# Optimization experiments

Hardware: AMD Instinct MI355X
Metric: run time of the kernel (lower is better)

The kernel has to match this reference:

```python
import jax, jax.numpy as jnp
import numpy as np

N_NODES = 50000
N_EDGES = 1600000
IN_FEAT = 128
HIDDEN = 128
CLASSES = 2


def gin_conv(x, src, dst, W, b, n_nodes):
    # GINConv (eps=0): h_i = mlp(x_i + sum_{j in N(i)} x_j)
    agg = jax.ops.segment_sum(x[src], dst, num_segments=n_nodes)  # [N, F]
    h = x + agg
    return h @ W + b


def setup_inputs() -> dict:
    key = jax.random.key(0)
    ks = jax.random.split(key, 8)
    x = jax.random.normal(ks[0], (N_NODES, IN_FEAT), dtype=jnp.float32)
    edge_index = jax.random.randint(ks[1], (2, N_EDGES), 0, N_NODES, dtype=jnp.int64)
    def lin(k, fan_in, fan_out):
        kw, kb = jax.random.split(k)
        bound = 1.0 / np.sqrt(fan_in)
        W = jax.random.uniform(kw, (fan_in, fan_out), jnp.float32, -bound, bound)
        b = jax.random.uniform(kb, (fan_out,), jnp.float32, -bound, bound)
        return W, b
    W1, b1 = lin(ks[2], IN_FEAT, HIDDEN)
    W2, b2 = lin(ks[3], HIDDEN, HIDDEN)
    W3, b3 = lin(ks[4], HIDDEN, CLASSES)
    return {"x": x, "edge_index": edge_index, "W1": W1, "b1": b1,
            "W2": W2, "b2": b2, "W3": W3, "b3": b3}


def reference(x, edge_index, W1, b1, W2, b2, W3, b3):
    src, dst = edge_index[0], edge_index[1]
    n = x.shape[0]
    h = jax.nn.relu(gin_conv(x, src, dst, W1, b1, n))
    h = jax.nn.relu(gin_conv(h, src, dst, W2, b2, n))
    return gin_conv(h, src, dst, W3, b3, n)
```

## Files before the change

kernel.cpp:

```cpp
#include <hip/hip_runtime.h>

#define NNODES 50000
#define NEDGES 1600000
#define F 128

#define NB 128
#define BSH 391
#define BCAP 13312
#define EPT 10

typedef __attribute__((ext_vector_type(8))) short bf16x8;
typedef __attribute__((ext_vector_type(4))) float f32x4;

__device__ inline unsigned short f2bf(float f) {
    union { float f; unsigned u; } v; v.f = f;
    unsigned r = v.u + 0x7FFF + ((v.u >> 16) & 1);
    return (unsigned short)(r >> 16);
}
__device__ inline float b2f(unsigned short h) {
    union { unsigned u; float f; } a;
    a.u = ((unsigned)h) << 16;
    return a.f;
}

__global__ __launch_bounds__(256) void cvt_bf16(const float4* __restrict__ in,
                                                ushort4* __restrict__ out, int n4) {
    int i = blockIdx.x * blockDim.x + threadIdx.x;
    int stride = gridDim.x * blockDim.x;
    for (; i < n4; i += stride) {
        float4 v = in[i];
        ushort4 o;
        o.x = f2bf(v.x); o.y = f2bf(v.y); o.z = f2bf(v.z); o.w = f2bf(v.w);
        out[i] = o;
    }
}

__global__ __launch_bounds__(256) void wprep2(const float* __restrict__ W1,
                                              const float* __restrict__ W2,
                                              unsigned short* __restrict__ Wf1,
                                              unsigned short* __restrict__ Wf2,
                                              int* __restrict__ gcnt) {
    int id = blockIdx.x * 256 + threadIdx.x;
    if (blockIdx.x == 0 && threadIdx.x < NB) gcnt[threadIdx.x] = 0;
    const float* W = (id < 2048) ? W1 : W2;
    unsigned short* Wf = (id < 2048) ? Wf1 : Wf2;
    id &= 2047;
    const int l = id & 63, nn = (id >> 6) & 7, s = id >> 9;
    const int c = nn * 16 + (l & 15);
    const int k0 = s * 32 + (l >> 4) * 8;
    ushort4 lo, hi;
    lo.x = f2bf(W[(k0 + 0) * F + c]); lo.y = f2bf(W[(k0 + 1) * F + c]);
    lo.z = f2bf(W[(k0 + 2) * F + c]); lo.w = f2bf(W[(k0 + 3) * F + c]);
    hi.x = f2bf(W[(k0 + 4) * F + c]); hi.y = f2bf(W[(k0 + 5) * F + c]);
    hi.z = f2bf(W[(k0 + 6) * F + c]); hi.w = f2bf(W[(k0 + 7) * F + c]);
    ushort4* p = (ushort4*)(Wf + (size_t)id * 8);
    p[0] = lo; p[1] = hi;
}

__global__ __launch_bounds__(256) void bucketA(const int* __restrict__ src,
                                               const int* __restrict__ dst,
                                               unsigned* __restrict__ E1,
                                               int* __restrict__ gcnt) {
    __shared__ unsigned hist[4][NB];
    __shared__ unsigned start[4][NB];
    const int t = threadIdx.x, w = t >> 6;
    for (int i = t; i < 4 * NB; i += 256) ((unsigned*)hist)[i] = 0;
    __syncthreads();
    const int base = blockIdx.x * (256 * EPT);
    unsigned rec[EPT]; int bkt[EPT]; unsigned rnk[EPT];
#pragma unroll
    for (int k = 0; k < EPT; ++k) {
        const int i = base + k * 256 + t;
        const int s = src[i], d = dst[i];
        const int b = d / BSH;
        rec[k] = ((unsigned)s << 9) | (unsigned)(d - b * BSH);
        bkt[k] = b;
        rnk[k] = atomicAdd(&hist[w][b], 1u);
    }
    __syncthreads();
    if (t < NB) {
        const unsigned h0 = hist[0][t], h1 = hist[1][t], h2 = hist[2][t], h3 = hist[3][t];
        const unsigned tot = h0 + h1 + h2 + h3;
        const unsigned g = tot ? (unsigned)atomicAdd(&gcnt[t], (int)tot) : 0u;
        start[0][t] = g;
        start[1][t] = g + h0;
        start[2][t] = g + h0 + h1;
        start[3][t] = g + h0 + h1 + h2;
    }
    __syncthreads();
#pragma unroll
    for (int k = 0; k < EPT; ++k) {
        const unsigned p = start[w][bkt[k]] + rnk[k];
        if (p < BCAP) E1[(size_t)bkt[k] * BCAP + p] = rec[k];
    }
}

__global__ __launch_bounds__(256) void bucketB(const unsigned* __restrict__ E1,
                                               const int* __restrict__ gcnt,
                                               int* __restrict__ off,
                                               unsigned short* __restrict__ ssrc) {
    __shared__ int cnt[BSH];
    __shared__ int cur[BSH];
    __shared__ int wtot[4];
    __shared__ int bst[NB];
    const int b = blockIdx.x, t = threadIdx.x;
    if (t < 64) {
        const int a0 = gcnt[t * 2], a1 = gcnt[t * 2 + 1];
        const int s = a0 + a1;
        int inc = s;
#pragma unroll
        for (int o = 1; o <= 32; o <<= 1) {
            int u = __shfl_up(inc, o);
            if (t >= o) inc += u;
        }
        bst[t * 2] = inc - s;
        bst[t * 2 + 1] = inc - s + a0;
    }
    for (int i = t; i < BSH; i += 256) cnt[i] = 0;
    __syncthreads();
    const int ne = min(gcnt[b], BCAP);
    const int ebase = bst[b];
    const unsigned* E = E1 + (size_t)b * BCAP;
    for (int i = t; i < ne; i += 256) atomicAdd(&cnt[E[i] & 511], 1);
    __syncthreads();
    const int i0 = t * 2, i1 = t * 2 + 1;
    const int a0 = (i0 < BSH) ? cnt[i0] : 0;
    const int a1 = (i1 < BSH) ? cnt[i1] : 0;
    const int s = a0 + a1;
    int inc = s;
    const int lane = t & 63, w = t >> 6;
#pragma unroll
    for (int o = 1; o <= 32; o <<= 1) {
        int u = __shfl_up(inc, o);
        if (lane >= o) inc += u;
    }
    if (lane == 63) wtot[w] = inc;
    __syncthreads();
    int woff = 0;
    for (int k = 0; k < w; ++k) woff += wtot[k];
    const int excl = woff + inc - s;
    if (i0 < BSH) {
        cur[i0] = excl;
        const int n = b * BSH + i0;
        if (n < NNODES) off[n] = ebase + excl;
    }
    if (i1 < BSH) {
        cur[i1] = excl + a0;
        const int n = b * BSH + i1;
        if (n < NNODES) off[n] = ebase + excl + a0;
    }
    if (b == NB - 1 && t == 0) off[NNODES] = NEDGES;
    __syncthreads();
    for (int i = t; i < ne; i += 256) {
        const unsigned rec = E[i];
        const int r = atomicAdd(&cur[rec & 511], 1);
        ssrc[ebase + r] = (unsigned short)(rec >> 9);
    }
}

__global__ __launch_bounds__(256) void agg_mlp(const unsigned short* __restrict__ h,
                                               const int* __restrict__ off,
                                               const unsigned short* __restrict__ ssrc,
                                               const unsigned short* __restrict__ Wfrag,
                                               const float* __restrict__ bias,
                                               unsigned short* __restrict__ out,
                                               int n, int relu) {
    __shared__ unsigned short Sl[4][16][128];
    const int w = threadIdx.x >> 6, lane = threadIdx.x & 63;
    const int nbase = blockIdx.x * 64 + w * 16;
    const int half = lane >> 5, l32 = lane & 31;

    for (int m = 0; m < 16; ++m) {
        const int node = nbase + m;
        float a0 = 0.f, a1 = 0.f, a2 = 0.f, a3 = 0.f;
        if (node < n) {
            const int e0 = off[node], e1 = off[node + 1];
            if (half == 0) {
                const ushort4 sv = *(const ushort4*)(h + (size_t)node * F + l32 * 4);
                a0 = b2f(sv.x); a1 = b2f(sv.y); a2 = b2f(sv.z); a3 = b2f(sv.w);
            }
            for (int eb = e0; eb < e1; eb += 64) {
                const int cnt = min(64, e1 - eb);
                const int myidx = (eb + lane < e1) ? (int)ssrc[eb + lane] : 0;
                int j = 0;
                for (; j + 8 <= cnt; j += 8) {
                    const int s0 = __shfl(myidx, j + 0 + half);
                    const int s1 = __shfl(myidx, j + 2 + half);
                    const int s2 = __shfl(myidx, j + 4 + half);
                    const int s3 = __shfl(myidx, j + 6 + half);
                    const ushort4 v0 = *(const ushort4*)(h + (size_t)s0 * F + l32 * 4);
                    const ushort4 v1 = *(const ushort4*)(h + (size_t)s1 * F + l32 * 4);
                    const ushort4 v2 = *(const ushort4*)(h + (size_t)s2 * F + l32 * 4);
                    const ushort4 v3 = *(const ushort4*)(h + (size_t)s3 * F + l32 * 4);
                    a0 += (b2f(v0.x) + b2f(v1.x)) + (b2f(v2.x) + b2f(v3.x));
                    a1 += (b2f(v0.y) + b2f(v1.y)) + (b2f(v2.y) + b2f(v3.y));
                    a2 += (b2f(v0.z) + b2f(v1.z)) + (b2f(v2.z) + b2f(v3.z));
                    a3 += (b2f(v0.w) + b2f(v1.w)) + (b2f(v2.w) + b2f(v3.w));
                }
                for (; j < cnt; j += 2) {
                    const int s = __shfl(myidx, min(j + half, cnt - 1));
                    if (j + half < cnt) {
                        const ushort4 v = *(const ushort4*)(h + (size_t)s * F + l32 * 4);
                        a0 += b2f(v.x); a1 += b2f(v.y); a2 += b2f(v.z); a3 += b2f(v.w);
                    }
                }
            }
        }
        a0 += __shfl_xor(a0, 32); a1 += __shfl_xor(a1, 32);
        a2 += __shfl_xor(a2, 32); a3 += __shfl_xor(a3, 32);
        if (half == 0) {
            ushort4 wbv;
            wbv.x = f2bf(a0); wbv.y = f2bf(a1); wbv.z = f2bf(a2); wbv.w = f2bf(a3);
            *(ushort4*)(&Sl[w][m][(l32 * 4) ^ ((m & 7) << 3)]) = wbv;
        }
    }

    const int r16 = lane & 15, hi = lane >> 4;
    f32x4 acc[8];
#pragma unroll
    for (int i = 0; i < 8; ++i) acc[i] = (f32x4){0.f, 0.f, 0.f, 0.f};
#pragma unroll
    for (int s = 0; s < 4; ++s) {
        const bf16x8 a = *(const bf16x8*)(&Sl[w][r16][(s * 32 + hi * 8) ^ ((r16 & 7) << 3)]);
#pragma unroll
        for (int nn = 0; nn < 8; ++nn) {
            const bf16x8 b = *(const bf16x8*)(Wfrag + ((size_t)(s * 8 + nn) * 64 + lane) * 8);
            acc[nn] = __builtin_amdgcn_mfma_f32_16x16x32_bf16(a, b, acc[nn], 0, 0, 0);
        }
    }
#pragma unroll
    for (int nn = 0; nn < 8; ++nn) {
        const int col = nn * 16 + r16;
        const float bv = bias[col];
#pragma unroll
        for (int r = 0; r < 4; ++r) {
            const int row = nbase + hi * 4 + r;
            if (row < n) {
                float v = acc[nn][r] + bv;
                if (relu) v = fmaxf(v, 0.f);
                out[(size_t)row * F + col] = f2bf(v);
            }
        }
    }
}

__global__ __launch_bounds__(256) void head_t(const unsigned short* __restrict__ Hb,
                                              const float4* __restrict__ W3,
                                              float2* __restrict__ y, int n) {
    const int wid = (blockIdx.x * blockDim.x + threadIdx.x) >> 6;
    const int lane = threadIdx.x & 63;
    if (wid >= n) return;
    const unsigned short* hp = Hb + (size_t)wid * F + lane * 2;
    const float hx = b2f(hp[0]), hy = b2f(hp[1]);
    const float4 w = W3[lane];
    float a0 = hx * w.x + hy * w.z;
    float a1 = hx * w.y + hy * w.w;
#pragma unroll
    for (int o = 32; o; o >>= 1) {
        a0 += __shfl_xor(a0, o);
        a1 += __shfl_xor(a1, o);
    }
    if (lane == 0) y[wid] = make_float2(a0, a1);
}

__global__ __launch_bounds__(256) void agg3(const float2* __restrict__ y,
                                            const int* __restrict__ off,
                                            const unsigned short* __restrict__ ssrc,
                                            const float* __restrict__ b3,
                                            float2* __restrict__ out, int n) {
    const int i = blockIdx.x * blockDim.x + threadIdx.x;
    if (i >= n) return;
    float2 acc = y[i];
    const int e1 = off[i + 1];
    for (int e = off[i]; e < e1; ++e) {
        const float2 v = y[ssrc[e]];
        acc.x += v.x;
        acc.y += v.y;
    }
    out[i] = make_float2(acc.x + b3[0], acc.y + b3[1]);
}

extern "C" void kernel_launch(void* const* d_in, const int* in_sizes, int n_in,
                              void* d_out, int out_size, void* d_ws, size_t ws_size,
                              hipStream_t stream) {
    const float* x  = (const float*)d_in[0];
    const int* ei   = (const int*)d_in[1];
    const int* src  = ei;
    const int* dst  = ei + NEDGES;
    const float* W1 = (const float*)d_in[2];
    const float* b1 = (const float*)d_in[3];
    const float* W2 = (const float*)d_in[4];
    const float* b2 = (const float*)d_in[5];
    const float* W3 = (const float*)d_in[6];
    const float* b3 = (const float*)d_in[7];
    float* out = (float*)d_out;

    char* ws = (char*)d_ws;
    const size_t featB = (size_t)NNODES * F * 2;
    unsigned short* xb = (unsigned short*)ws;
    unsigned short* Hb = (unsigned short*)(ws + featB);
    char* p = ws + 2 * featB;
    float* y3 = (float*)p;                 p += (size_t)NNODES * 2 * 4 + 256;
    unsigned short* Wf1 = (unsigned short*)p; p += 2048 * 8 * 2;
    unsigned short* Wf2 = (unsigned short*)p; p += 2048 * 8 * 2;
    unsigned* E1 = (unsigned*)p;           p += (size_t)NB * BCAP * 4;
    int* gcnt = (int*)p;                   p += NB * 4 + 256;
    int* off = (int*)p;                    p += (size_t)(NNODES + 1) * 4 + 256;
    unsigned short* ssrc = (unsigned short*)p;

    cvt_bf16<<<1024, 256, 0, stream>>>((const float4*)x, (ushort4*)xb, NNODES * F / 4);
    wprep2<<<16, 256, 0, stream>>>(W1, W2, Wf1, Wf2, gcnt);

    bucketA<<<NEDGES / (256 * EPT), 256, 0, stream>>>(src, dst, E1, gcnt);
    bucketB<<<NB, 256, 0, stream>>>(E1, gcnt, off, ssrc);

    const int fusedBlocks = (NNODES + 63) / 64;

    agg_mlp<<<fusedBlocks, 256, 0, stream>>>(xb, off, ssrc, Wf1, b1, Hb, NNODES, 1);
    agg_mlp<<<fusedBlocks, 256, 0, stream>>>(Hb, off, ssrc, Wf2, b2, xb, NNODES, 1);

    head_t<<<(NNODES + 3) / 4, 256, 0, stream>>>(xb, (const float4*)W3, (float2*)y3, NNODES);
    agg3<<<(NNODES + 255) / 256, 256, 0, stream>>>((const float2*)y3, off, ssrc, b3, (float2*)out, NNODES);
}
```

Measured before the change: 315.7 us.

## Split wavefront halves across two nodes and use single-wave blocks in agg_mlp

Each 64-lane wave now aggregates two nodes at once, one per 32-lane half, instead of splitting one node's edges between the halves and reducing them with a cross-half shuffle. The inner gather loop is unrolled to 8 loads per half, and blocks shrink to one wave covering 16 nodes, so there are four times as many blocks. The aim is to drop the cross-half reduction and wasted tail lanes, raise memory-level parallelism and balance the load at finer grain. In exchange, the two halves can diverge when their nodes have different degrees, and register use rises from the wider unroll.

```diff
diff --git a/kernel.cpp b/kernel.cpp
--- a/kernel.cpp
+++ b/kernel.cpp
@@ -158,61 +158,66 @@
     }
 }
 
-__global__ __launch_bounds__(256) void agg_mlp(const unsigned short* __restrict__ h,
-                                               const int* __restrict__ off,
-                                               const unsigned short* __restrict__ ssrc,
-                                               const unsigned short* __restrict__ Wfrag,
-                                               const float* __restrict__ bias,
-                                               unsigned short* __restrict__ out,
-                                               int n, int relu) {
-    __shared__ unsigned short Sl[4][16][128];
-    const int w = threadIdx.x >> 6, lane = threadIdx.x & 63;
-    const int nbase = blockIdx.x * 64 + w * 16;
+__global__ __launch_bounds__(64) void agg_mlp(const unsigned short* __restrict__ h,
+                                              const int* __restrict__ off,
+                                              const unsigned short* __restrict__ ssrc,
+                                              const unsigned short* __restrict__ Wfrag,
+                                              const float* __restrict__ bias,
+                                              unsigned short* __restrict__ out,
+                                              int n, int relu) {
+    __shared__ unsigned short Sl[16][128];
+    const int lane = threadIdx.x;
+    const int nbase = blockIdx.x * 16;
     const int half = lane >> 5, l32 = lane & 31;
 
-    for (int m = 0; m < 16; ++m) {
-        const int node = nbase + m;
+    for (int m = 0; m < 16; m += 2) {
+        const int row = m + half;
+        const int node = nbase + row;
         float a0 = 0.f, a1 = 0.f, a2 = 0.f, a3 = 0.f;
         if (node < n) {
             const int e0 = off[node], e1 = off[node + 1];
-            if (half == 0) {
-                const ushort4 sv = *(const ushort4*)(h + (size_t)node * F + l32 * 4);
-                a0 = b2f(sv.x); a1 = b2f(sv.y); a2 = b2f(sv.z); a3 = b2f(sv.w);
-            }
-            for (int eb = e0; eb < e1; eb += 64) {
-                const int cnt = min(64, e1 - eb);
-                const int myidx = (eb + lane < e1) ? (int)ssrc[eb + lane] : 0;
+            const ushort4 sv = *(const ushort4*)(h + (size_t)node * F + l32 * 4);
+            a0 = b2f(sv.x); a1 = b2f(sv.y); a2 = b2f(sv.z); a3 = b2f(sv.w);
+            for (int eb = e0; eb < e1; eb += 32) {
+                const int cnt = min(32, e1 - eb);
+                const int myidx = (eb + l32 < e1) ? (int)ssrc[eb + l32] : 0;
                 int j = 0;
                 for (; j + 8 <= cnt; j += 8) {
-                    const int s0 = __shfl(myidx, j + 0 + half);
-                    const int s1 = __shfl(myidx, j + 2 + half);
-                    const int s2 = __shfl(myidx, j + 4 + half);
-                    const int s3 = __shfl(myidx, j + 6 + half);
+                    const int s0 = __shfl(myidx, j + 0, 32);
+                    const int s1 = __shfl(myidx, j + 1, 32);
+                    const int s2 = __shfl(myidx, j + 2, 32);
+                    const int s3 = __shfl(myidx, j + 3, 32);
+                    const int s4 = __shfl(myidx, j + 4, 32);
+                    const int s5 = __shfl(myidx, j + 5, 32);
+                    const int s6 = __shfl(myidx, j + 6, 32);
+                    const int s7 = __shfl(myidx, j + 7, 32);
                     const ushort4 v0 = *(const ushort4*)(h + (size_t)s0 * F + l32 * 4);
                     const ushort4 v1 = *(const ushort4*)(h + (size_t)s1 * F + l32 * 4);
                     const ushort4 v2 = *(const ushort4*)(h + (size_t)s2 * F + l32 * 4);
                     const ushort4 v3 = *(const ushort4*)(h + (size_t)s3 * F + l32 * 4);
-                    a0 += (b2f(v0.x) + b2f(v1.x)) + (b2f(v2.x) + b2f(v3.x));
-                    a1 += (b2f(v0.y) + b2f(v1.y)) + (b2f(v2.y) + b2f(v3.y));
-                    a2 += (b2f(v0.z) + b2f(v1.z)) + (b2f(v2.z) + b2f(v3.z));
-                    a3 += (b2f(v0.w) + b2f(v1.w)) + (b2f(v2.w) + b2f(v3.w));
+                    const ushort4 v4 = *(const ushort4*)(h + (size_t)s4 * F + l32 * 4);
+                    const ushort4 v5 = *(const ushort4*)(h + (size_t)s5 * F + l32 * 4);
+                    const ushort4 v6 = *(const ushort4*)(h + (size_t)s6 * F + l32 * 4);
+                    const ushort4 v7 = *(const ushort4*)(h + (size_t)s7 * F + l32 * 4);
+                    a0 += ((b2f(v0.x) + b2f(v1.x)) + (b2f(v2.x) + b2f(v3.x))) +
+                          ((b2f(v4.x) + b2f(v5.x)) + (b2f(v6.x) + b2f(v7.x)));
+                    a1 += ((b2f(v0.y) + b2f(v1.y)) + (b2f(v2.y) + b2f(v3.y))) +
+                          ((b2f(v4.y) + b2f(v5.y)) + (b2f(v6.y) + b2f(v7.y)));
+                    a2 += ((b2f(v0.z) + b2f(v1.z)) + (b2f(v2.z) + b2f(v3.z))) +
+                          ((b2f(v4.z) + b2f(v5.z)) + (b2f(v6.z) + b2f(v7.z)));
+                    a3 += ((b2f(v0.w) + b2f(v1.w)) + (b2f(v2.w) + b2f(v3.w))) +
+                          ((b2f(v4.w) + b2f(v5.w)) + (b2f(v6.w) + b2f(v7.w)));
                 }
-                for (; j < cnt; j += 2) {
-                    const int s = __shfl(myidx, min(j + half, cnt - 1));
-                    if (j + half < cnt) {
-                        const ushort4 v = *(const ushort4*)(h + (size_t)s * F + l32 * 4);
-                        a0 += b2f(v.x); a1 += b2f(v.y); a2 += b2f(v.z); a3 += b2f(v.w);
-                    }
+                for (; j < cnt; ++j) {
+                    const int s = __shfl(myidx, j, 32);
+                    const ushort4 v = *(const ushort4*)(h + (size_t)s * F + l32 * 4);
+                    a0 += b2f(v.x); a1 += b2f(v.y); a2 += b2f(v.z); a3 += b2f(v.w);
                 }
             }
         }
-        a0 += __shfl_xor(a0, 32); a1 += __shfl_xor(a1, 32);
-        a2 += __shfl_xor(a2, 32); a3 += __shfl_xor(a3, 32);
-        if (half == 0) {
-            ushort4 wbv;
-            wbv.x = f2bf(a0); wbv.y = f2bf(a1); wbv.z = f2bf(a2); wbv.w = f2bf(a3);
-            *(ushort4*)(&Sl[w][m][(l32 * 4) ^ ((m & 7) << 3)]) = wbv;
-        }
+        ushort4 wbv;
+        wbv.x = f2bf(a0); wbv.y = f2bf(a1); wbv.z = f2bf(a2); wbv.w = f2bf(a3);
+        *(ushort4*)(&Sl[row][(l32 * 4) ^ ((row & 7) << 3)]) = wbv;
     }
 
     const int r16 = lane & 15, hi = lane >> 4;
@@ -221,7 +226,7 @@
     for (int i = 0; i < 8; ++i) acc[i] = (f32x4){0.f, 0.f, 0.f, 0.f};
 #pragma unroll
     for (int s = 0; s < 4; ++s) {
-        const bf16x8 a = *(const bf16x8*)(&Sl[w][r16][(s * 32 + hi * 8) ^ ((r16 & 7) << 3)]);
+        const bf16x8 a = *(const bf16x8*)(&Sl[r16][(s * 32 + hi * 8) ^ ((r16 & 7) << 3)]);
 #pragma unroll
         for (int nn = 0; nn < 8; ++nn) {
             const bf16x8 b = *(const bf16x8*)(Wfrag + ((size_t)(s * 8 + nn) * 64 + lane) * 8);
@@ -314,10 +319,10 @@
     bucketA<<<NEDGES / (256 * EPT), 256, 0, stream>>>(src, dst, E1, gcnt);
     bucketB<<<NB, 256, 0, stream>>>(E1, gcnt, off, ssrc);
 
-    const int fusedBlocks = (NNODES + 63) / 64;
-
-    agg_mlp<<<fusedBlocks, 256, 0, stream>>>(xb, off, ssrc, Wf1, b1, Hb, NNODES, 1);
-    agg_mlp<<<fusedBlocks, 256, 0, stream>>>(Hb, off, ssrc, Wf2, b2, xb, NNODES, 1);
+    const int fusedBlocks = (NNODES + 15) / 16;
+
+    agg_mlp<<<fusedBlocks, 64, 0, stream>>>(xb, off, ssrc, Wf1, b1, Hb, NNODES, 1);
+    agg_mlp<<<fusedBlocks, 64, 0, stream>>>(Hb, off, ssrc, Wf2, b2, xb, NNODES, 1);
 
     head_t<<<(NNODES + 3) / 4, 256, 0, stream>>>(xb, (const float4*)W3, (float2*)y3, NNODES);
     agg3<<<(NNODES + 255) / 256, 256, 0, stream>>>((const float2*)y3, off, ssrc, b3, (float2*)out, NNODES);
```

After: 314.1 us. About the same (-0.5%).
